# Performance work log

Measured on AMD Instinct MI355X. Metric: run time of the kernel, lower is better.

## Reference

```python
import jax, jax.numpy as jnp
import numpy as np

# irreps_in = 128x0e + 64x1o + 32x2e -> (multiplicity, 2l+1) blocks
IRREPS = [(128, 1), (64, 3), (32, 5)]
DIM = sum(m * d for m, d in IRREPS)  # 480
EPS = 1e-8


def setup_inputs() -> dict:
    key = jax.random.key(0)
    features = jax.random.normal(key, (100000, DIM), dtype=jnp.float32)
    return {"features": features}


def reference(features) -> jnp.ndarray:
    batch = features.shape[:-1]
    out_blocks = []
    off = 0
    for mul, d in IRREPS:  # fixed small structural loop over irrep types
        block = features[..., off:off + mul * d].reshape(*batch, mul, d)
        # per-irrep L2 norm over the (2l+1) components -> (..., mul)
        norms = jnp.sqrt(jnp.sum(block * block, axis=-1))
        eps_norms = jnp.maximum(norms, EPS)
        scalings = jax.nn.silu(eps_norms) / eps_norms
        out_blocks.append((block * scalings[..., None]).reshape(*batch, mul * d))
        off += mul * d
    return jnp.concatenate(out_blocks, axis=-1)
```

## Files before the change

kernel.cpp:

```cpp
#include <hip/hip_runtime.h>
#include <math.h>

#define ROWS_PER_BLOCK 8
#define DIM 480
#define NGROUPS 224
#define NV4 120
#define BLOCK 256

__global__ __launch_bounds__(BLOCK) void norm_act_kernel(
    const float* __restrict__ in, float* __restrict__ out, int n_rows)
{
    __shared__ float sdata[ROWS_PER_BLOCK * DIM];
    __shared__ float sscal[ROWS_PER_BLOCK * NGROUPS];

    const int tid  = threadIdx.x;
    const int row0 = blockIdx.x * ROWS_PER_BLOCK;
    const int rows = min(ROWS_PER_BLOCK, n_rows - row0);
    const int nv4  = rows * NV4;

    const float4* gin  = (const float4*)(in  + (size_t)row0 * DIM);
    float4*       gout = (float4*)      (out + (size_t)row0 * DIM);

    for (int v = tid; v < nv4; v += BLOCK) {
        ((float4*)sdata)[v] = gin[v];
    }
    __syncthreads();

    const int ng = rows * NGROUPS;
    for (int g = tid; g < ng; g += BLOCK) {
        const int row = g / NGROUPS;
        const int gi  = g - row * NGROUPS;
        const float* base = sdata + row * DIM;
        float ss;
        if (gi < 128) {
            const float x = base[gi];
            ss = x * x;
        } else if (gi < 192) {
            const float* p = base + 128 + (gi - 128) * 3;
            ss = p[0]*p[0] + p[1]*p[1] + p[2]*p[2];
        } else {
            const float* p = base + 320 + (gi - 192) * 5;
            ss = p[0]*p[0] + p[1]*p[1] + p[2]*p[2] + p[3]*p[3] + p[4]*p[4];
        }
        float n = sqrtf(ss);
        n = fmaxf(n, 1e-8f);
        sscal[row * NGROUPS + gi] = 1.0f / (1.0f + __expf(-n));
    }
    __syncthreads();

    for (int v = tid; v < nv4; v += BLOCK) {
        const int row = v / NV4;
        const int c4  = v - row * NV4;
        const int e0  = c4 * 4;
        float4 x = ((const float4*)sdata)[v];
        const float* sc = sscal + row * NGROUPS;
        float s[4];
        #pragma unroll
        for (int k = 0; k < 4; ++k) {
            const int e = e0 + k;
            int gidx;
            if (e < 128)       gidx = e;
            else if (e < 320)  gidx = 128 + (e - 128) / 3;
            else               gidx = 192 + (e - 320) / 5;
            s[k] = sc[gidx];
        }
        x.x *= s[0]; x.y *= s[1]; x.z *= s[2]; x.w *= s[3];
        gout[v] = x;
    }
}

extern "C" void kernel_launch(void* const* d_in, const int* in_sizes, int n_in,
                              void* d_out, int out_size, void* d_ws, size_t ws_size,
                              hipStream_t stream) {
    const float* in  = (const float*)d_in[0];
    float*       out = (float*)d_out;
    const int n_rows = in_sizes[0] / DIM;
    const int grid   = (n_rows + ROWS_PER_BLOCK - 1) / ROWS_PER_BLOCK;
    norm_act_kernel<<<grid, BLOCK, 0, stream>>>(in, out, n_rows);
}
```

Baseline: 324.0 us.

## Drop shared-memory staging; assign each thread whole irrep groups in registers

Replaces the three-phase shared-memory kernel (load, per-group norms, scale) with a flat grid where each thread owns 4 irreps of a single type and loads them straight into registers as float4s. Scalars use |x| directly, and vectors and tensors compute their norms from 12 or 20 contiguous floats. This removes the LDS round trip, both barriers and the per-element division-based index mapping. It also adds nontemporal stores and a hardware reciprocal for the sigmoid, at the cost of less coalesced access within the vector and tensor segments, since each lane strides 48 or 80 bytes.

```diff
diff --git a/kernel.cpp b/kernel.cpp
--- a/kernel.cpp
+++ b/kernel.cpp
@@ -1,71 +1,74 @@
 #include <hip/hip_runtime.h>
 #include <math.h>
 
-#define ROWS_PER_BLOCK 8
 #define DIM 480
-#define NGROUPS 224
-#define NV4 120
 #define BLOCK 256
+#define EPS 1e-8f
+
+typedef float v4 __attribute__((ext_vector_type(4)));
+
+__device__ __forceinline__ float sig(float n) {
+    n = fmaxf(n, EPS);
+    return __builtin_amdgcn_rcpf(1.0f + __expf(-n));
+}
 
 __global__ __launch_bounds__(BLOCK) void norm_act_kernel(
     const float* __restrict__ in, float* __restrict__ out, int n_rows)
 {
-    __shared__ float sdata[ROWS_PER_BLOCK * DIM];
-    __shared__ float sscal[ROWS_PER_BLOCK * NGROUPS];
+    const int tid = blockIdx.x * BLOCK + threadIdx.x;
+    const int t0 = n_rows * 32;
+    const int t1 = n_rows * 16;
+    const int t2 = n_rows * 8;
 
-    const int tid  = threadIdx.x;
-    const int row0 = blockIdx.x * ROWS_PER_BLOCK;
-    const int rows = min(ROWS_PER_BLOCK, n_rows - row0);
-    const int nv4  = rows * NV4;
-
-    const float4* gin  = (const float4*)(in  + (size_t)row0 * DIM);
-    float4*       gout = (float4*)      (out + (size_t)row0 * DIM);
-
-    for (int v = tid; v < nv4; v += BLOCK) {
-        ((float4*)sdata)[v] = gin[v];
-    }
-    __syncthreads();
-
-    const int ng = rows * NGROUPS;
-    for (int g = tid; g < ng; g += BLOCK) {
-        const int row = g / NGROUPS;
-        const int gi  = g - row * NGROUPS;
-        const float* base = sdata + row * DIM;
-        float ss;
-        if (gi < 128) {
-            const float x = base[gi];
-            ss = x * x;
-        } else if (gi < 192) {
-            const float* p = base + 128 + (gi - 128) * 3;
-            ss = p[0]*p[0] + p[1]*p[1] + p[2]*p[2];
-        } else {
-            const float* p = base + 320 + (gi - 192) * 5;
-            ss = p[0]*p[0] + p[1]*p[1] + p[2]*p[2] + p[3]*p[3] + p[4]*p[4];
-        }
-        float n = sqrtf(ss);
-        n = fmaxf(n, 1e-8f);
-        sscal[row * NGROUPS + gi] = 1.0f / (1.0f + __expf(-n));
-    }
-    __syncthreads();
-
-    for (int v = tid; v < nv4; v += BLOCK) {
-        const int row = v / NV4;
-        const int c4  = v - row * NV4;
-        const int e0  = c4 * 4;
-        float4 x = ((const float4*)sdata)[v];
-        const float* sc = sscal + row * NGROUPS;
-        float s[4];
-        #pragma unroll
-        for (int k = 0; k < 4; ++k) {
-            const int e = e0 + k;
-            int gidx;
-            if (e < 128)       gidx = e;
-            else if (e < 320)  gidx = 128 + (e - 128) / 3;
-            else               gidx = 192 + (e - 320) / 5;
-            s[k] = sc[gidx];
-        }
-        x.x *= s[0]; x.y *= s[1]; x.z *= s[2]; x.w *= s[3];
-        gout[v] = x;
+    if (tid < t0) {
+        const int row = tid >> 5, j = tid & 31;
+        const size_t off = (size_t)row * DIM + j * 4;
+        v4 x = *(const v4*)(in + off);
+        x.x *= sig(fabsf(x.x));
+        x.y *= sig(fabsf(x.y));
+        x.z *= sig(fabsf(x.z));
+        x.w *= sig(fabsf(x.w));
+        __builtin_nontemporal_store(x, (v4*)(out + off));
+    } else if (tid < t0 + t1) {
+        const int t = tid - t0;
+        const int row = t >> 4, j = t & 15;
+        const size_t off = (size_t)row * DIM + 128 + j * 12;
+        v4 a = *(const v4*)(in + off);
+        v4 b = *(const v4*)(in + off + 4);
+        v4 c = *(const v4*)(in + off + 8);
+        const float s0 = sig(sqrtf(a.x*a.x + a.y*a.y + a.z*a.z));
+        const float s1 = sig(sqrtf(a.w*a.w + b.x*b.x + b.y*b.y));
+        const float s2 = sig(sqrtf(b.z*b.z + b.w*b.w + c.x*c.x));
+        const float s3 = sig(sqrtf(c.y*c.y + c.z*c.z + c.w*c.w));
+        a.x *= s0; a.y *= s0; a.z *= s0;
+        a.w *= s1; b.x *= s1; b.y *= s1;
+        b.z *= s2; b.w *= s2; c.x *= s2;
+        c.y *= s3; c.z *= s3; c.w *= s3;
+        __builtin_nontemporal_store(a, (v4*)(out + off));
+        __builtin_nontemporal_store(b, (v4*)(out + off + 4));
+        __builtin_nontemporal_store(c, (v4*)(out + off + 8));
+    } else if (tid < t0 + t1 + t2) {
+        const int t = tid - t0 - t1;
+        const int row = t >> 3, j = t & 7;
+        const size_t off = (size_t)row * DIM + 320 + j * 20;
+        v4 a = *(const v4*)(in + off);
+        v4 b = *(const v4*)(in + off + 4);
+        v4 c = *(const v4*)(in + off + 8);
+        v4 d = *(const v4*)(in + off + 12);
+        v4 e = *(const v4*)(in + off + 16);
+        const float s0 = sig(sqrtf(a.x*a.x + a.y*a.y + a.z*a.z + a.w*a.w + b.x*b.x));
+        const float s1 = sig(sqrtf(b.y*b.y + b.z*b.z + b.w*b.w + c.x*c.x + c.y*c.y));
+        const float s2 = sig(sqrtf(c.z*c.z + c.w*c.w + d.x*d.x + d.y*d.y + d.z*d.z));
+        const float s3 = sig(sqrtf(d.w*d.w + e.x*e.x + e.y*e.y + e.z*e.z + e.w*e.w));
+        a.x *= s0; a.y *= s0; a.z *= s0; a.w *= s0; b.x *= s0;
+        b.y *= s1; b.z *= s1; b.w *= s1; c.x *= s1; c.y *= s1;
+        c.z *= s2; c.w *= s2; d.x *= s2; d.y *= s2; d.z *= s2;
+        d.w *= s3; e.x *= s3; e.y *= s3; e.z *= s3; e.w *= s3;
+        __builtin_nontemporal_store(a, (v4*)(out + off));
+        __builtin_nontemporal_store(b, (v4*)(out + off + 4));
+        __builtin_nontemporal_store(c, (v4*)(out + off + 8));
+        __builtin_nontemporal_store(d, (v4*)(out + off + 12));
+        __builtin_nontemporal_store(e, (v4*)(out + off + 16));
     }
 }
 
@@ -74,7 +77,8 @@
                               hipStream_t stream) {
     const float* in  = (const float*)d_in[0];
     float*       out = (float*)d_out;
-    const int n_rows = in_sizes[0] / DIM;
-    const int grid   = (n_rows + ROWS_PER_BLOCK - 1) / ROWS_PER_BLOCK;
+    const int n_rows  = in_sizes[0] / DIM;
+    const int threads = n_rows * (32 + 16 + 8);
+    const int grid    = (threads + BLOCK - 1) / BLOCK;
     norm_act_kernel<<<grid, BLOCK, 0, stream>>>(in, out, n_rows);
 }
```

After: 393.3 us. 1.21x slower.
